# Kernel optimization log

Measured on AMD Instinct MI355X. Metric: run time of the kernel, lower is better.

The kernel has to match this reference:

```python
import jax, jax.numpy as jnp
import numpy as np

DIR_EDGES = [(0,1),(0,2),(0,3),(0,4),(0,13),(0,15),(3,5),(5,6),(4,7),(7,8),(1,9),(9,10),(2,11),(11,12),(13,14),(15,16)]
BP_EDGES = [(1,0),(1,2),(1,3),(1,4),(1,5)]
BODY_PARTS = [[13,14,15,16],[0,3,4],[1,9,10],[2,11,12],[5,6],[7,8]]
V1, V2 = 17, 6           # dir-vec graph nodes, body-part graph nodes
F1 = 16                  # st_gcn output channels
MAX_BP = 4               # max_body_part_edges
NOISE_DIM = 64
EPS = 1e-5


def build_A(num_node, edges, max_hop=2, center=0):
    """ST-GCN 'spatial' partition strategy -> (2*max_hop+1, V, V) float32."""
    adj = np.zeros((num_node, num_node))
    for i, j in edges:
        adj[i, j] = 1.0
        adj[j, i] = 1.0
    hop_dis = np.full((num_node, num_node), np.inf)
    powers = [np.linalg.matrix_power(adj + np.eye(num_node), d) for d in range(max_hop + 1)]
    arrive = np.stack(powers) > 0
    for d in range(max_hop, -1, -1):
        hop_dis[arrive[d]] = d
    adjacency = np.zeros((num_node, num_node))
    for hop in range(max_hop + 1):
        adjacency[hop_dis == hop] = 1.0
    Dl = adjacency.sum(0)
    Dn = np.zeros((num_node, num_node))
    for i in range(num_node):
        if Dl[i] > 0:
            Dn[i, i] = Dl[i] ** -1
    na = adjacency @ Dn
    parts = []
    for hop in range(max_hop + 1):
        a_root = np.zeros((num_node, num_node))
        a_close = np.zeros_like(a_root)
        a_far = np.zeros_like(a_root)
        for i in range(num_node):
            for j in range(num_node):
                if hop_dis[j, i] == hop:
                    if hop_dis[j, center] == hop_dis[i, center]:
                        a_root[j, i] = na[j, i]
                    elif hop_dis[j, center] > hop_dis[i, center]:
                        a_close[j, i] = na[j, i]
                    else:
                        a_far[j, i] = na[j, i]
        if hop == 0:
            parts.append(a_root)
        else:
            parts.append(a_root + a_close)
            parts.append(a_far)
    return np.stack(parts).astype(np.float32)


def _bn_params(k, c):
    k1, k2, k3, k4 = jax.random.split(k, 4)
    gamma = 1.0 + 0.1 * jax.random.normal(k1, (c,), dtype=jnp.float32)
    beta = 0.1 * jax.random.normal(k2, (c,), dtype=jnp.float32)
    mean = 0.1 * jax.random.normal(k3, (c,), dtype=jnp.float32)
    var = 1.0 + 0.1 * jax.random.uniform(k4, (c,), dtype=jnp.float32)
    return gamma, beta, mean, var


def setup_inputs() -> dict:
    key = jax.random.key(0)
    ks = jax.random.split(key, 12)
    n, t = 16, 2048
    poses = jax.random.normal(ks[0], (n, t, V1 * 3), dtype=jnp.float32)
    A1 = jnp.asarray(build_A(V1, DIR_EDGES, max_hop=2, center=0))  # (5,17,17)
    A2 = jnp.asarray(build_A(V2, BP_EDGES, max_hop=2, center=0))   # (5,6,6)
    K = 5
    w1 = 0.05 * jax.random.normal(ks[1], (F1 * K, 3, 9, 5), dtype=jnp.float32)
    b1 = 0.05 * jax.random.normal(ks[2], (F1 * K,), dtype=jnp.float32)
    w2 = 0.05 * jax.random.normal(ks[3], (F1 * K, MAX_BP * F1, 9, 3), dtype=jnp.float32)
    b2 = 0.05 * jax.random.normal(ks[4], (F1 * K,), dtype=jnp.float32)
    w3 = 0.05 * jax.random.normal(ks[5], (16, F1 * V2, 5), dtype=jnp.float32)
    b3 = 0.05 * jax.random.normal(ks[6], (16,), dtype=jnp.float32)
    w4 = 0.05 * jax.random.normal(ks[7], (NOISE_DIM, 16, 3), dtype=jnp.float32)
    b4 = 0.05 * jax.random.normal(ks[8], (NOISE_DIM,), dtype=jnp.float32)
    g1, be1, m1, v1 = _bn_params(ks[9], F1 * V1)
    g2, be2, m2, v2 = _bn_params(ks[10], F1 * V2)
    kk = jax.random.split(ks[11], 2)
    g3, be3, m3, v3 = _bn_params(kk[0], 16)
    g4, be4, m4, v4 = _bn_params(kk[1], NOISE_DIM)
    return dict(poses=poses, A1=A1, A2=A2, w1=w1, b1=b1, g1=g1, be1=be1, m1=m1, v1=v1,
                w2=w2, b2=b2, g2=g2, be2=be2, m2=m2, v2=v2,
                w3=w3, b3=b3, g3=g3, be3=be3, m3=m3, v3=v3,
                w4=w4, b4=b4, g4=g4, be4=be4, m4=m4, v4=v4)


def _bn(x, g, b, m, v):
    # x: (n, C, t), eval-mode BatchNorm1d
    s = (g * jax.lax.rsqrt(v + EPS))
    return (x - m[None, :, None]) * s[None, :, None] + b[None, :, None]


def _conv2d(x, w, b, pad):
    y = jax.lax.conv_general_dilated(x, w, (1, 1), [(pad[0], pad[0]), (pad[1], pad[1])],
                                     dimension_numbers=('NCHW', 'OIHW', 'NCHW'))
    return y + b[None, :, None, None]


def _conv1d(x, w, b, pad):
    y = jax.lax.conv_general_dilated(x, w, (1,), [(pad, pad)],
                                     dimension_numbers=('NCH', 'OIH', 'NCH'))
    return y + b[None, :, None]


def _leaky(x):
    return jax.nn.leaky_relu(x, 0.01)


def reference(poses, A1, A2, w1, b1, g1, be1, m1, v1, w2, b2, g2, be2, m2, v2,
              w3, b3, g3, be3, m3, v3, w4, b4, g4, be4, m4, v4):
    n, t, _ = poses.shape
    K = A1.shape[0]
    # (n, 3, t, V1)
    x = jnp.transpose(poses.reshape(n, t, V1, 3), (0, 3, 1, 2))
    # st_gcn1: 2D conv over (t, v) then graph-partition einsum
    y = _conv2d(x, w1, b1, (4, 2)).reshape(n, K, F1, t, V1)
    f1 = jnp.einsum('nkctv,kvw->nctw', y, A1)            # (n, F1, t, V1)
    # bn1 on flattened (F1*V1) channels
    z = jnp.transpose(f1, (0, 1, 3, 2)).reshape(n, F1 * V1, t)
    z = _bn(z, g1, be1, m1, v1)
    f1bn = jnp.transpose(z.reshape(n, F1, V1, t), (0, 1, 3, 2))  # (n, F1, t, V1)
    # body-part gather/pad assembly -> (n, t, MAX_BP*F1, V2)
    cols = []
    for idxs in BODY_PARTS:
        g = f1bn[:, :, :, jnp.asarray(idxs)]             # (n, F1, t, L)
        g = jnp.transpose(g, (0, 2, 1, 3)).reshape(n, t, -1)  # (n, t, F1*L)
        cols.append(jnp.pad(g, ((0, 0), (0, 0), (0, MAX_BP * F1 - g.shape[-1]))))
    f2_in = jnp.transpose(jnp.stack(cols, axis=-1), (0, 2, 1, 3))  # (n, 64, t, V2)
    # st_gcn2
    y2 = _conv2d(f2_in, w2, b2, (4, 1)).reshape(n, K, F1, t, V2)
    f2 = jnp.einsum('nkctv,kvw->nctw', y2, A2)           # (n, F1, t, V2)
    z2 = jnp.transpose(f2, (0, 1, 3, 2)).reshape(n, F1 * V2, t)
    z2 = _bn(z2, g2, be2, m2, v2)
    f2bn = jnp.transpose(z2.reshape(n, F1, V2, t), (0, 1, 3, 2))   # (n, F1, t, V2)
    # (n, F1*V2, t)
    f3_in = jnp.transpose(jnp.transpose(f2bn, (0, 2, 1, 3)).reshape(n, t, -1), (0, 2, 1))
    f3 = _leaky(_bn(_conv1d(f3_in, w3, b3, 2), g3, be3, m3, v3))
    f4 = _leaky(_bn(_conv1d(f3, w4, b4, 1), g4, be4, m4, v4))
    return jnp.transpose(f4, (0, 2, 1))                  # (n, t, noise_dim)
```

## Files before the change

### kernel.cpp

```cpp
#include <hip/hip_runtime.h>
#include <stdint.h>

typedef unsigned short u16;
typedef __attribute__((ext_vector_type(8))) __bf16 bf16x8;
typedef __attribute__((ext_vector_type(8))) u16 u16x8;
typedef __attribute__((ext_vector_type(4))) float f32x4;

#define T_LEN 2048
#define NB 16

__device__ __forceinline__ u16 f2bf(float f){
  uint32_t x = __builtin_bit_cast(uint32_t, f);
  x += 0x7FFFu + ((x >> 16) & 1u);
  return (u16)(x >> 16);
}

__constant__ int c_part[17] = {1,2,3,1,1,4,4,5,5,2,2,3,3,0,0,0,0};
__constant__ int c_pidx[17] = {0,0,0,1,2,0,1,0,1,1,2,1,2,0,1,2,3};
__constant__ int c_plen[17] = {3,3,3,3,3,2,2,2,2,3,3,3,3,4,4,4,4};

__global__ void prep_all(
  const float* __restrict__ w1, const float* __restrict__ A1, const float* __restrict__ g1, const float* __restrict__ v1, u16* __restrict__ W1f,
  const float* __restrict__ w2, const float* __restrict__ A2, const float* __restrict__ g2, const float* __restrict__ v2, u16* __restrict__ W2f,
  const float* __restrict__ w3, const float* __restrict__ g3, const float* __restrict__ v3, u16* __restrict__ W3f,
  const float* __restrict__ w4, const float* __restrict__ g4, const float* __restrict__ v4, u16* __restrict__ W4f,
  const float* b1, const float* be1, const float* m1,
  const float* b2, const float* be2, const float* m2,
  const float* b3, const float* be3, const float* m3,
  const float* b4, const float* be4, const float* m4,
  float* bias1f, float* bias2f, float* bias3f, float* bias4f)
{
  const int bid = blockIdx.x;
  if (bid < 544){
    int idx = bid * 256 + threadIdx.x;
    int cw = idx >> 9, kp = idx & 511;
    int c = cw / 17, w = cw - c * 17;
    int dt = kp / 56, r0 = kp - dt * 56;
    float val = 0.f;
    if (dt < 9 && r0 < 51){
      int u = r0 / 3, ci = r0 - u * 3;
      for (int kk = 0; kk < 5; ++kk)
        for (int dv = 0; dv < 5; ++dv){
          int v = u - dv + 2;
          if (v >= 0 && v < 17)
            val += w1[(kk*16 + c)*135 + ci*45 + dt*5 + dv] * A1[kk*289 + v*17 + w];
        }
      val *= g1[cw] * rsqrtf(v1[cw] + 1e-5f);
    }
    int mt = cw >> 4, r = cw & 15, ks = kp >> 5, kq = kp & 31;
    W1f[(ks*17 + mt)*512 + ((kq>>3)*16 + r)*8 + (kq&7)] = f2bf(val);
  } else if (bid < 1480){
    int idx = (bid - 544) * 256 + threadIdx.x;
    int cw = idx / 2496, kp = idx - cw * 2496;
    int c = cw / 6, w = cw - c * 6;
    int dt = kp / 272, fj = kp - dt * 272;
    float val = 0.f;
    if (dt < 9){
      int f = fj / 17, J = fj - f * 17;
      int p = c_part[J];
      int ci = f * c_plen[J] + c_pidx[J];
      for (int kk = 0; kk < 5; ++kk)
        for (int dv = 0; dv < 3; ++dv){
          int v = p - dv + 1;
          if (v >= 0 && v < 6)
            val += w2[(kk*16 + c)*1728 + ci*27 + dt*3 + dv] * A2[kk*36 + v*6 + w];
        }
      val *= g2[cw] * rsqrtf(v2[cw] + 1e-5f);
    }
    int mt = cw >> 4, r = cw & 15, ks = kp >> 5, kq = kp & 31;
    W2f[(ks*6 + mt)*512 + ((kq>>3)*16 + r)*8 + (kq&7)] = f2bf(val);
  } else {
    int idx = (bid - 1480) * 256 + threadIdx.x;
    if (idx < 8192){
      int cw = idx >> 9, kp = idx & 511;
      int dt = kp / 96, ch = kp - dt * 96;
      float val = 0.f;
      if (dt < 5){
        float s = g3[cw] * rsqrtf(v3[cw] + 1e-5f);
        val = s * w3[cw*480 + ch*5 + dt];
      }
      int ks = kp >> 5, kq = kp & 31;
      W3f[ks*512 + ((kq>>3)*16 + cw)*8 + (kq&7)] = f2bf(val);
    } else if (idx < 12288){
      int i2 = idx - 8192;
      int cw = i2 >> 6, kp = i2 & 63;
      int dt = kp >> 4, ch = kp & 15;
      float val = 0.f;
      if (dt < 3){
        float s = g4[cw] * rsqrtf(v4[cw] + 1e-5f);
        val = s * w4[cw*48 + ch*3 + dt];
      }
      int mt = cw >> 4, r = cw & 15, ks = kp >> 5, kq = kp & 31;
      W4f[(ks*4 + mt)*512 + ((kq>>3)*16 + r)*8 + (kq&7)] = f2bf(val);
    } else if (idx < 12736){
      int tid = idx - 12288;
      if (tid < 272){
        int c = tid / 17, w = tid - c * 17;
        float beff = 0.f;
        for (int kk = 0; kk < 5; ++kk){
          float rs = 0.f;
          for (int v = 0; v < 17; ++v) rs += A1[kk*289 + v*17 + w];
          beff += b1[kk*16 + c] * rs;
        }
        float s = g1[tid] * rsqrtf(v1[tid] + 1e-5f);
        bias1f[tid] = s * (beff - m1[tid]) + be1[tid];
      } else if (tid < 368){
        int cw = tid - 272;
        int c = cw / 6, w = cw - c * 6;
        float beff = 0.f;
        for (int kk = 0; kk < 5; ++kk){
          float rs = 0.f;
          for (int v = 0; v < 6; ++v) rs += A2[kk*36 + v*6 + w];
          beff += b2[kk*16 + c] * rs;
        }
        float s = g2[cw] * rsqrtf(v2[cw] + 1e-5f);
        bias2f[cw] = s * (beff - m2[cw]) + be2[cw];
      } else if (tid < 384){
        int o = tid - 368;
        float s = g3[o] * rsqrtf(v3[o] + 1e-5f);
        bias3f[o] = s * (b3[o] - m3[o]) + be3[o];
      } else if (tid < 448){
        int o = tid - 384;
        float s = g4[o] * rsqrtf(v4[o] + 1e-5f);
        bias4f[o] = s * (b4[o] - m4[o]) + be4[o];
      }
    }
  }
}

template<int MT, int NW, int NM, int KSTEPS, int RD, int PITCH, int SRC_R, bool IN_F32>
__launch_bounds__(NW*64)
__global__ void gemm_big(const void* __restrict__ src, const u16* __restrict__ Wf,
                         const float* __restrict__ bias, u16* __restrict__ dst)
{
  constexpr int MTOT = MT * 16;
  constexpr int ROWS = 76;
  constexpr int NTH = NW * 64;
  __shared__ u16 patch[ROWS * PITCH];
  const int t0 = blockIdx.x * 64;
  const int n  = blockIdx.y;
  const int tid = threadIdx.x;

  if constexpr (IN_F32){
    for (int idx = tid; idx < ROWS * PITCH; idx += NTH){
      int row = idx / PITCH, col = idx - row * PITCH;
      int ts = t0 + row - 4;
      u16 v = 0;
      if (ts >= 0 && ts < T_LEN && col < SRC_R)
        v = f2bf(((const float*)src)[((size_t)n * T_LEN + ts) * SRC_R + col]);
      patch[idx] = v;
    }
  } else {
    constexpr int GP = PITCH / 8;
    for (int idx = tid; idx < ROWS * GP; idx += NTH){
      int row = idx / GP, g = idx - row * GP;
      int ts = t0 + row - 4;
      int col = g * 8;
      u16x8 v = (u16x8)0;
      if (ts >= 0 && ts < T_LEN && col + 8 <= SRC_R)
        v = *reinterpret_cast<const u16x8*>(&((const u16*)src)[((size_t)n * T_LEN + ts) * SRC_R + col]);
      *reinterpret_cast<u16x8*>(&patch[row * PITCH + col]) = v;
    }
  }
  __syncthreads();

  const int lane = tid & 63;
  const int h    = tid >> 6;
  const int q    = lane >> 4;
  const int l15  = lane & 15;

  bool mok[NM];
  const u16* aptr[NM];
#pragma unroll
  for (int i = 0; i < NM; ++i){
    int mt = h * NM + i;
    mok[i] = (mt < MT);
    aptr[i] = Wf + (size_t)(mok[i] ? mt : 0) * 512 + lane * 8;
  }
  const u16* bp[4];
#pragma unroll
  for (int j = 0; j < 4; ++j)
    bp[j] = patch + (j * 16 + l15) * PITCH;

  f32x4 acc[NM][4];
#pragma unroll
  for (int i = 0; i < NM; ++i)
#pragma unroll
    for (int j = 0; j < 4; ++j)
      acc[i][j] = (f32x4){0.f, 0.f, 0.f, 0.f};

  bf16x8 aF[2][NM];
  bf16x8 bF[2][4];

  auto loadA = [&](int buf, int ks){
    const size_t so = (size_t)ks * (MT * 512);
#pragma unroll
    for (int i = 0; i < NM; ++i)
      aF[buf][i] = *reinterpret_cast<const bf16x8*>(aptr[i] + so);
  };
  auto loadB = [&](int buf, int ks){
    const int k0 = ks * 32 + q * 8;
    const int dt = k0 / RD;
    const int r  = k0 - dt * RD;
    const int od = dt * PITCH + r;
#pragma unroll
    for (int j = 0; j < 4; ++j)
      bF[buf][j] = *reinterpret_cast<const bf16x8*>(bp[j] + od);
  };
  auto step = [&](int buf){
#pragma unroll
    for (int i = 0; i < NM; ++i){
      if (!mok[i]) continue;
#pragma unroll
      for (int j = 0; j < 4; ++j)
        acc[i][j] = __builtin_amdgcn_mfma_f32_16x16x32_bf16(aF[buf][i], bF[buf][j], acc[i][j], 0, 0, 0);
    }
  };

  loadA(0, 0); loadB(0, 0);
  for (int ks = 0; ks + 2 <= KSTEPS; ks += 2){
    loadA(1, ks + 1); loadB(1, ks + 1);
    step(0);
    if (ks + 2 < KSTEPS){ loadA(0, ks + 2); loadB(0, ks + 2); }
    step(1);
  }

#pragma unroll
  for (int i = 0; i < NM; ++i){
    if (!mok[i]) continue;
    const int chb = (h * NM + i) * 16 + q * 4;
    const float b0 = bias[chb+0], b1v = bias[chb+1], b2v = bias[chb+2], b3v = bias[chb+3];
#pragma unroll
    for (int j = 0; j < 4; ++j){
      const int t = t0 + j * 16 + l15;
      ushort4 o;
      o.x = f2bf(acc[i][j][0] + b0);
      o.y = f2bf(acc[i][j][1] + b1v);
      o.z = f2bf(acc[i][j][2] + b2v);
      o.w = f2bf(acc[i][j][3] + b3v);
      *reinterpret_cast<ushort4*>(&dst[((size_t)n * T_LEN + t) * MTOT + chb]) = o;
    }
  }
}

__launch_bounds__(256)
__global__ void gemm34(const u16* __restrict__ X2, const u16* __restrict__ W3f,
                       const float* __restrict__ bias3, const u16* __restrict__ W4f,
                       const float* __restrict__ bias4, float* __restrict__ out)
{
  __shared__ u16 patch[86 * 104];
  __shared__ u16 X3L[80 * 16];
  const int t0 = blockIdx.x * 64;
  const int n  = blockIdx.y;
  const int tid = threadIdx.x;

  for (int idx = tid; idx < 86 * 13; idx += 256){
    int row = idx / 13, g = idx - row * 13;
    int ts = t0 + row - 10;
    int col = g * 8;
    u16x8 v = (u16x8)0;
    if (ts >= 0 && ts < T_LEN && col + 8 <= 96)
      v = *reinterpret_cast<const u16x8*>(&X2[((size_t)n * T_LEN + ts) * 96 + col]);
    *reinterpret_cast<u16x8*>(&patch[row * 104 + col]) = v;
  }
  __syncthreads();

  const int lane = tid & 63;
  const int wv   = tid >> 6;
  const int q    = lane >> 4;
  const int l15  = lane & 15;

  {
    const bool two = (wv == 0);
    f32x4 a0 = (f32x4){0,0,0,0}, a1 = (f32x4){0,0,0,0};
    bf16x8 aF[2], b0F[2], b1F[2];
    const u16* bp0 = patch + (16 * wv + l15) * 104;
    const u16* bp1 = patch + (64 + l15) * 104;
    auto load3 = [&](int buf, int ks){
      const int k0 = ks * 32 + q * 8;
      const int dt = k0 / 96, r = k0 - dt * 96;
      const int od = dt * 104 + r;
      aF[buf]  = *reinterpret_cast<const bf16x8*>(W3f + ks * 512 + lane * 8);
      b0F[buf] = *reinterpret_cast<const bf16x8*>(bp0 + od);
      b1F[buf] = *reinterpret_cast<const bf16x8*>(bp1 + od);
    };
    auto step3 = [&](int buf){
      a0 = __builtin_amdgcn_mfma_f32_16x16x32_bf16(aF[buf], b0F[buf], a0, 0, 0, 0);
      if (two) a1 = __builtin_amdgcn_mfma_f32_16x16x32_bf16(aF[buf], b1F[buf], a1, 0, 0, 0);
    };
    load3(0, 0);
    for (int ks = 0; ks + 2 <= 16; ks += 2){
      load3(1, ks + 1);
      step3(0);
      if (ks + 2 < 16) load3(0, ks + 2);
      step3(1);
    }
    const float c0 = bias3[q*4+0], c1 = bias3[q*4+1], c2 = bias3[q*4+2], c3 = bias3[q*4+3];
    {
      int trow = 16 * wv + l15;
      int t = t0 - 8 + trow;
      float v0 = a0[0]+c0, v1 = a0[1]+c1, v2 = a0[2]+c2, v3 = a0[3]+c3;
      v0 = v0 > 0.f ? v0 : 0.01f*v0; v1 = v1 > 0.f ? v1 : 0.01f*v1;
      v2 = v2 > 0.f ? v2 : 0.01f*v2; v3 = v3 > 0.f ? v3 : 0.01f*v3;
      if (t < 0 || t >= T_LEN){ v0 = v1 = v2 = v3 = 0.f; }
      ushort4 o; o.x = f2bf(v0); o.y = f2bf(v1); o.z = f2bf(v2); o.w = f2bf(v3);
      *reinterpret_cast<ushort4*>(&X3L[trow * 16 + q * 4]) = o;
    }
    if (two){
      int trow = 64 + l15;
      int t = t0 - 8 + trow;
      float v0 = a1[0]+c0, v1 = a1[1]+c1, v2 = a1[2]+c2, v3 = a1[3]+c3;
      v0 = v0 > 0.f ? v0 : 0.01f*v0; v1 = v1 > 0.f ? v1 : 0.01f*v1;
      v2 = v2 > 0.f ? v2 : 0.01f*v2; v3 = v3 > 0.f ? v3 : 0.01f*v3;
      if (t < 0 || t >= T_LEN){ v0 = v1 = v2 = v3 = 0.f; }
      ushort4 o; o.x = f2bf(v0); o.y = f2bf(v1); o.z = f2bf(v2); o.w = f2bf(v3);
      *reinterpret_cast<ushort4*>(&X3L[trow * 16 + q * 4]) = o;
    }
  }
  __syncthreads();

  {
    f32x4 acc[4];
#pragma unroll
    for (int j = 0; j < 4; ++j) acc[j] = (f32x4){0,0,0,0};
    bf16x8 aF[2], bF[2][4];
    auto load4 = [&](int buf, int ks){
      const int k0 = ks * 32 + q * 8;
      const int dt2 = k0 >> 4, ch0 = k0 & 15;
      aF[buf] = *reinterpret_cast<const bf16x8*>(W4f + (ks * 4 + wv) * 512 + lane * 8);
#pragma unroll
      for (int j = 0; j < 4; ++j)
        bF[buf][j] = *reinterpret_cast<const bf16x8*>(&X3L[(j * 16 + l15 + dt2 + 7) * 16 + ch0]);
    };
    load4(0, 0); load4(1, 1);
#pragma unroll
    for (int j = 0; j < 4; ++j)
      acc[j] = __builtin_amdgcn_mfma_f32_16x16x32_bf16(aF[0], bF[0][j], acc[j], 0, 0, 0);
#pragma unroll
    for (int j = 0; j < 4; ++j)
      acc[j] = __builtin_amdgcn_mfma_f32_16x16x32_bf16(aF[1], bF[1][j], acc[j], 0, 0, 0);

    const int chb = wv * 16 + q * 4;
    const float c0 = bias4[chb+0], c1 = bias4[chb+1], c2 = bias4[chb+2], c3 = bias4[chb+3];
#pragma unroll
    for (int j = 0; j < 4; ++j){
      const int t = t0 + j * 16 + l15;
      float v0 = acc[j][0]+c0, v1 = acc[j][1]+c1, v2 = acc[j][2]+c2, v3 = acc[j][3]+c3;
      v0 = v0 > 0.f ? v0 : 0.01f*v0; v1 = v1 > 0.f ? v1 : 0.01f*v1;
      v2 = v2 > 0.f ? v2 : 0.01f*v2; v3 = v3 > 0.f ? v3 : 0.01f*v3;
      float4 o; o.x = v0; o.y = v1; o.z = v2; o.w = v3;
      *reinterpret_cast<float4*>(&out[((size_t)n * T_LEN + t) * 64 + chb]) = o;
    }
  }
}

extern "C" void kernel_launch(void* const* d_in, const int* in_sizes, int n_in,
                              void* d_out, int out_size, void* d_ws, size_t ws_size,
                              hipStream_t stream)
{
  const float* poses = (const float*)d_in[0];
  const float* A1  = (const float*)d_in[1];
  const float* A2  = (const float*)d_in[2];
  const float* w1  = (const float*)d_in[3];
  const float* b1  = (const float*)d_in[4];
  const float* g1  = (const float*)d_in[5];
  const float* be1 = (const float*)d_in[6];
  const float* m1  = (const float*)d_in[7];
  const float* v1  = (const float*)d_in[8];
  const float* w2  = (const float*)d_in[9];
  const float* b2  = (const float*)d_in[10];
  const float* g2  = (const float*)d_in[11];
  const float* be2 = (const float*)d_in[12];
  const float* m2  = (const float*)d_in[13];
  const float* v2  = (const float*)d_in[14];
  const float* w3  = (const float*)d_in[15];
  const float* b3  = (const float*)d_in[16];
  const float* g3  = (const float*)d_in[17];
  const float* be3 = (const float*)d_in[18];
  const float* m3  = (const float*)d_in[19];
  const float* v3  = (const float*)d_in[20];
  const float* w4  = (const float*)d_in[21];
  const float* b4  = (const float*)d_in[22];
  const float* g4  = (const float*)d_in[23];
  const float* be4 = (const float*)d_in[24];
  const float* m4  = (const float*)d_in[25];
  const float* v4  = (const float*)d_in[26];

  uint8_t* ws = (uint8_t*)d_ws;
  size_t off = 0;
  auto alloc = [&](size_t bytes) -> void* {
    void* p = ws + off;
    off += (bytes + 255) & ~(size_t)255;
    return p;
  };
  u16* W1f = (u16*)alloc(16 * 17 * 512 * 2);
  u16* W2f = (u16*)alloc(78 * 6 * 512 * 2);
  u16* W3f = (u16*)alloc(16 * 1 * 512 * 2);
  u16* W4f = (u16*)alloc(2 * 4 * 512 * 2);
  float* bias1f = (float*)alloc(272 * 4);
  float* bias2f = (float*)alloc(96 * 4);
  float* bias3f = (float*)alloc(16 * 4);
  float* bias4f = (float*)alloc(64 * 4);
  u16* X1 = (u16*)alloc((size_t)NB * T_LEN * 272 * 2);
  u16* X2 = (u16*)alloc((size_t)NB * T_LEN * 96 * 2);

  hipLaunchKernelGGL(prep_all, dim3(1530), dim3(256), 0, stream,
                     w1, A1, g1, v1, W1f,
                     w2, A2, g2, v2, W2f,
                     w3, g3, v3, W3f,
                     w4, g4, v4, W4f,
                     b1, be1, m1, b2, be2, m2, b3, be3, m3, b4, be4, m4,
                     bias1f, bias2f, bias3f, bias4f);

  dim3 grid(T_LEN / 64, NB);
  hipLaunchKernelGGL((gemm_big<17, 6, 3, 16, 56, 56, 51, true>), grid, dim3(384), 0, stream,
                     (const void*)poses, W1f, bias1f, X1);
  hipLaunchKernelGGL((gemm_big<6, 3, 2, 78, 272, 280, 272, false>), grid, dim3(192), 0, stream,
                     (const void*)X1, W2f, bias2f, X2);
  hipLaunchKernelGGL(gemm34, grid, dim3(256), 0, stream, X2, W3f, bias3f, W4f, bias4f, (float*)d_out);
}
```

Before: 173.1 us.

## Split GEMM output channels across grid z and halve gemm34 time tile

Replaces the templated gemm_big with two specialized kernels that split output-channel tiles across a new grid z dimension, which doubles the block count and gives each wave fewer M tiles. Stage 2 now computes one M tile per wave with a triple-buffered fragment pipeline. gemm34 uses 32-step time tiles, so it launches twice as many blocks with smaller shared memory. The patch row count is trimmed to the rows actually read. The aim is more parallelism and occupancy, at the cost of each input patch being loaded and converted redundantly by both z blocks.

```diff
diff --git a/kernel.cpp b/kernel.cpp
--- a/kernel.cpp
+++ b/kernel.cpp
@@ -128,39 +128,24 @@
   }
 }
 
-template<int MT, int NW, int NM, int KSTEPS, int RD, int PITCH, int SRC_R, bool IN_F32>
-__launch_bounds__(NW*64)
-__global__ void gemm_big(const void* __restrict__ src, const u16* __restrict__ Wf,
-                         const float* __restrict__ bias, u16* __restrict__ dst)
+__launch_bounds__(192)
+__global__ void gemm_s1(const float* __restrict__ src, const u16* __restrict__ Wf,
+                        const float* __restrict__ bias, u16* __restrict__ dst)
 {
-  constexpr int MTOT = MT * 16;
-  constexpr int ROWS = 76;
-  constexpr int NTH = NW * 64;
+  constexpr int KSTEPS = 16, RD = 56, PITCH = 56, SRC_R = 51, ROWS = 73, NM = 3;
   __shared__ u16 patch[ROWS * PITCH];
   const int t0 = blockIdx.x * 64;
   const int n  = blockIdx.y;
+  const int z  = blockIdx.z;
   const int tid = threadIdx.x;
 
-  if constexpr (IN_F32){
-    for (int idx = tid; idx < ROWS * PITCH; idx += NTH){
-      int row = idx / PITCH, col = idx - row * PITCH;
-      int ts = t0 + row - 4;
-      u16 v = 0;
-      if (ts >= 0 && ts < T_LEN && col < SRC_R)
-        v = f2bf(((const float*)src)[((size_t)n * T_LEN + ts) * SRC_R + col]);
-      patch[idx] = v;
-    }
-  } else {
-    constexpr int GP = PITCH / 8;
-    for (int idx = tid; idx < ROWS * GP; idx += NTH){
-      int row = idx / GP, g = idx - row * GP;
-      int ts = t0 + row - 4;
-      int col = g * 8;
-      u16x8 v = (u16x8)0;
-      if (ts >= 0 && ts < T_LEN && col + 8 <= SRC_R)
-        v = *reinterpret_cast<const u16x8*>(&((const u16*)src)[((size_t)n * T_LEN + ts) * SRC_R + col]);
-      *reinterpret_cast<u16x8*>(&patch[row * PITCH + col]) = v;
-    }
+  for (int idx = tid; idx < ROWS * PITCH; idx += 192){
+    int row = idx / PITCH, col = idx - row * PITCH;
+    int ts = t0 + row - 4;
+    u16 v = 0;
+    if (ts >= 0 && ts < T_LEN && col < SRC_R)
+      v = f2bf(src[((size_t)n * T_LEN + ts) * SRC_R + col]);
+    patch[idx] = v;
   }
   __syncthreads();
 
@@ -173,8 +158,8 @@
   const u16* aptr[NM];
 #pragma unroll
   for (int i = 0; i < NM; ++i){
-    int mt = h * NM + i;
-    mok[i] = (mt < MT);
+    int mt = z * 9 + h * 3 + i;
+    mok[i] = (mt < 17);
     aptr[i] = Wf + (size_t)(mok[i] ? mt : 0) * 512 + lane * 8;
   }
   const u16* bp[4];
@@ -192,13 +177,11 @@
   bf16x8 aF[2][NM];
   bf16x8 bF[2][4];
 
-  auto loadA = [&](int buf, int ks){
-    const size_t so = (size_t)ks * (MT * 512);
+  auto loadstep = [&](int buf, int ks){
+    const size_t so = (size_t)ks * (17 * 512);
 #pragma unroll
     for (int i = 0; i < NM; ++i)
       aF[buf][i] = *reinterpret_cast<const bf16x8*>(aptr[i] + so);
-  };
-  auto loadB = [&](int buf, int ks){
     const int k0 = ks * 32 + q * 8;
     const int dt = k0 / RD;
     const int r  = k0 - dt * RD;
@@ -217,18 +200,18 @@
     }
   };
 
-  loadA(0, 0); loadB(0, 0);
+  loadstep(0, 0);
   for (int ks = 0; ks + 2 <= KSTEPS; ks += 2){
-    loadA(1, ks + 1); loadB(1, ks + 1);
+    loadstep(1, ks + 1);
     step(0);
-    if (ks + 2 < KSTEPS){ loadA(0, ks + 2); loadB(0, ks + 2); }
+    if (ks + 2 < KSTEPS) loadstep(0, ks + 2);
     step(1);
   }
 
 #pragma unroll
   for (int i = 0; i < NM; ++i){
     if (!mok[i]) continue;
-    const int chb = (h * NM + i) * 16 + q * 4;
+    const int chb = (z * 9 + h * 3 + i) * 16 + q * 4;
     const float b0 = bias[chb+0], b1v = bias[chb+1], b2v = bias[chb+2], b3v = bias[chb+3];
 #pragma unroll
     for (int j = 0; j < 4; ++j){
@@ -238,8 +221,91 @@
       o.y = f2bf(acc[i][j][1] + b1v);
       o.z = f2bf(acc[i][j][2] + b2v);
       o.w = f2bf(acc[i][j][3] + b3v);
-      *reinterpret_cast<ushort4*>(&dst[((size_t)n * T_LEN + t) * MTOT + chb]) = o;
-    }
+      *reinterpret_cast<ushort4*>(&dst[((size_t)n * T_LEN + t) * 272 + chb]) = o;
+    }
+  }
+}
+
+__launch_bounds__(192)
+__global__ void gemm_s2(const u16* __restrict__ src, const u16* __restrict__ Wf,
+                        const float* __restrict__ bias, u16* __restrict__ dst)
+{
+  constexpr int KSTEPS = 78, RD = 272, PITCH = 280, SRC_R = 272, ROWS = 73;
+  __shared__ u16 patch[ROWS * PITCH];
+  const int t0 = blockIdx.x * 64;
+  const int n  = blockIdx.y;
+  const int z  = blockIdx.z;
+  const int tid = threadIdx.x;
+
+  constexpr int GP = SRC_R / 8;
+  for (int idx = tid; idx < ROWS * GP; idx += 192){
+    int row = idx / GP, g = idx - row * GP;
+    int ts = t0 + row - 4;
+    int col = g * 8;
+    u16x8 v = (u16x8)0;
+    if (ts >= 0 && ts < T_LEN)
+      v = *reinterpret_cast<const u16x8*>(&src[((size_t)n * T_LEN + ts) * SRC_R + col]);
+    *reinterpret_cast<u16x8*>(&patch[row * PITCH + col]) = v;
+  }
+  __syncthreads();
+
+  const int lane = tid & 63;
+  const int h    = tid >> 6;
+  const int q    = lane >> 4;
+  const int l15  = lane & 15;
+  const int mt   = z * 3 + h;
+
+  const u16* aptr = Wf + (size_t)mt * 512 + lane * 8;
+  const u16* bp[4];
+#pragma unroll
+  for (int j = 0; j < 4; ++j)
+    bp[j] = patch + (j * 16 + l15) * PITCH;
+
+  f32x4 acc[4];
+#pragma unroll
+  for (int j = 0; j < 4; ++j) acc[j] = (f32x4){0.f, 0.f, 0.f, 0.f};
+
+  bf16x8 aF[3];
+  bf16x8 bF[3][4];
+
+  auto loadstep = [&](int buf, int ks){
+    aF[buf] = *reinterpret_cast<const bf16x8*>(aptr + (size_t)ks * (6 * 512));
+    const int k0 = ks * 32 + q * 8;
+    const int dt = k0 / RD;
+    const int r  = k0 - dt * RD;
+    const int od = dt * PITCH + r;
+#pragma unroll
+    for (int j = 0; j < 4; ++j)
+      bF[buf][j] = *reinterpret_cast<const bf16x8*>(bp[j] + od);
+  };
+  auto step = [&](int buf){
+#pragma unroll
+    for (int j = 0; j < 4; ++j)
+      acc[j] = __builtin_amdgcn_mfma_f32_16x16x32_bf16(aF[buf], bF[buf][j], acc[j], 0, 0, 0);
+  };
+
+  loadstep(0, 0);
+  loadstep(1, 1);
+  for (int ks = 0; ks < KSTEPS; ks += 3){
+    loadstep(2, ks + 2);
+    step(0);
+    if (ks + 3 < KSTEPS) loadstep(0, ks + 3);
+    step(1);
+    if (ks + 4 < KSTEPS) loadstep(1, ks + 4);
+    step(2);
+  }
+
+  const int chb = mt * 16 + q * 4;
+  const float b0 = bias[chb+0], b1v = bias[chb+1], b2v = bias[chb+2], b3v = bias[chb+3];
+#pragma unroll
+  for (int j = 0; j < 4; ++j){
+    const int t = t0 + j * 16 + l15;
+    ushort4 o;
+    o.x = f2bf(acc[j][0] + b0);
+    o.y = f2bf(acc[j][1] + b1v);
+    o.z = f2bf(acc[j][2] + b2v);
+    o.w = f2bf(acc[j][3] + b3v);
+    *reinterpret_cast<ushort4*>(&dst[((size_t)n * T_LEN + t) * 96 + chb]) = o;
   }
 }
 
@@ -248,18 +314,18 @@
                        const float* __restrict__ bias3, const u16* __restrict__ W4f,
                        const float* __restrict__ bias4, float* __restrict__ out)
 {
-  __shared__ u16 patch[86 * 104];
-  __shared__ u16 X3L[80 * 16];
-  const int t0 = blockIdx.x * 64;
+  __shared__ u16 patch[53 * 104];
+  __shared__ u16 X3L[48 * 16];
+  const int t0 = blockIdx.x * 32;
   const int n  = blockIdx.y;
   const int tid = threadIdx.x;
 
-  for (int idx = tid; idx < 86 * 13; idx += 256){
-    int row = idx / 13, g = idx - row * 13;
+  for (int idx = tid; idx < 53 * 12; idx += 256){
+    int row = idx / 12, g = idx - row * 12;
     int ts = t0 + row - 10;
     int col = g * 8;
     u16x8 v = (u16x8)0;
-    if (ts >= 0 && ts < T_LEN && col + 8 <= 96)
+    if (ts >= 0 && ts < T_LEN)
       v = *reinterpret_cast<const u16x8*>(&X2[((size_t)n * T_LEN + ts) * 96 + col]);
     *reinterpret_cast<u16x8*>(&patch[row * 104 + col]) = v;
   }
@@ -270,80 +336,60 @@
   const int q    = lane >> 4;
   const int l15  = lane & 15;
 
-  {
-    const bool two = (wv == 0);
-    f32x4 a0 = (f32x4){0,0,0,0}, a1 = (f32x4){0,0,0,0};
-    bf16x8 aF[2], b0F[2], b1F[2];
+  if (wv < 3){
+    f32x4 a0 = (f32x4){0,0,0,0};
+    bf16x8 aF[2], bF[2];
     const u16* bp0 = patch + (16 * wv + l15) * 104;
-    const u16* bp1 = patch + (64 + l15) * 104;
     auto load3 = [&](int buf, int ks){
       const int k0 = ks * 32 + q * 8;
       const int dt = k0 / 96, r = k0 - dt * 96;
-      const int od = dt * 104 + r;
-      aF[buf]  = *reinterpret_cast<const bf16x8*>(W3f + ks * 512 + lane * 8);
-      b0F[buf] = *reinterpret_cast<const bf16x8*>(bp0 + od);
-      b1F[buf] = *reinterpret_cast<const bf16x8*>(bp1 + od);
-    };
-    auto step3 = [&](int buf){
-      a0 = __builtin_amdgcn_mfma_f32_16x16x32_bf16(aF[buf], b0F[buf], a0, 0, 0, 0);
-      if (two) a1 = __builtin_amdgcn_mfma_f32_16x16x32_bf16(aF[buf], b1F[buf], a1, 0, 0, 0);
+      aF[buf] = *reinterpret_cast<const bf16x8*>(W3f + ks * 512 + lane * 8);
+      bF[buf] = *reinterpret_cast<const bf16x8*>(bp0 + dt * 104 + r);
     };
     load3(0, 0);
     for (int ks = 0; ks + 2 <= 16; ks += 2){
       load3(1, ks + 1);
-      step3(0);
+      a0 = __builtin_amdgcn_mfma_f32_16x16x32_bf16(aF[0], bF[0], a0, 0, 0, 0);
       if (ks + 2 < 16) load3(0, ks + 2);
-      step3(1);
+      a0 = __builtin_amdgcn_mfma_f32_16x16x32_bf16(aF[1], bF[1], a0, 0, 0, 0);
     }
     const float c0 = bias3[q*4+0], c1 = bias3[q*4+1], c2 = bias3[q*4+2], c3 = bias3[q*4+3];
-    {
-      int trow = 16 * wv + l15;
-      int t = t0 - 8 + trow;
-      float v0 = a0[0]+c0, v1 = a0[1]+c1, v2 = a0[2]+c2, v3 = a0[3]+c3;
-      v0 = v0 > 0.f ? v0 : 0.01f*v0; v1 = v1 > 0.f ? v1 : 0.01f*v1;
-      v2 = v2 > 0.f ? v2 : 0.01f*v2; v3 = v3 > 0.f ? v3 : 0.01f*v3;
-      if (t < 0 || t >= T_LEN){ v0 = v1 = v2 = v3 = 0.f; }
-      ushort4 o; o.x = f2bf(v0); o.y = f2bf(v1); o.z = f2bf(v2); o.w = f2bf(v3);
-      *reinterpret_cast<ushort4*>(&X3L[trow * 16 + q * 4]) = o;
-    }
-    if (two){
-      int trow = 64 + l15;
-      int t = t0 - 8 + trow;
-      float v0 = a1[0]+c0, v1 = a1[1]+c1, v2 = a1[2]+c2, v3 = a1[3]+c3;
-      v0 = v0 > 0.f ? v0 : 0.01f*v0; v1 = v1 > 0.f ? v1 : 0.01f*v1;
-      v2 = v2 > 0.f ? v2 : 0.01f*v2; v3 = v3 > 0.f ? v3 : 0.01f*v3;
-      if (t < 0 || t >= T_LEN){ v0 = v1 = v2 = v3 = 0.f; }
-      ushort4 o; o.x = f2bf(v0); o.y = f2bf(v1); o.z = f2bf(v2); o.w = f2bf(v3);
-      *reinterpret_cast<ushort4*>(&X3L[trow * 16 + q * 4]) = o;
-    }
+    int trow = 16 * wv + l15;
+    int t = t0 - 8 + trow;
+    float v0 = a0[0]+c0, v1 = a0[1]+c1, v2 = a0[2]+c2, v3 = a0[3]+c3;
+    v0 = v0 > 0.f ? v0 : 0.01f*v0; v1 = v1 > 0.f ? v1 : 0.01f*v1;
+    v2 = v2 > 0.f ? v2 : 0.01f*v2; v3 = v3 > 0.f ? v3 : 0.01f*v3;
+    if (t < 0 || t >= T_LEN){ v0 = v1 = v2 = v3 = 0.f; }
+    ushort4 o; o.x = f2bf(v0); o.y = f2bf(v1); o.z = f2bf(v2); o.w = f2bf(v3);
+    *reinterpret_cast<ushort4*>(&X3L[trow * 16 + q * 4]) = o;
   }
   __syncthreads();
 
   {
-    f32x4 acc[4];
-#pragma unroll
-    for (int j = 0; j < 4; ++j) acc[j] = (f32x4){0,0,0,0};
-    bf16x8 aF[2], bF[2][4];
+    f32x4 acc[2];
+#pragma unroll
+    for (int j = 0; j < 2; ++j) acc[j] = (f32x4){0,0,0,0};
+    bf16x8 aF[2], bF[2][2];
     auto load4 = [&](int buf, int ks){
       const int k0 = ks * 32 + q * 8;
       const int dt2 = k0 >> 4, ch0 = k0 & 15;
       aF[buf] = *reinterpret_cast<const bf16x8*>(W4f + (ks * 4 + wv) * 512 + lane * 8);
 #pragma unroll
-      for (int j = 0; j < 4; ++j)
+      for (int j = 0; j < 2; ++j)
         bF[buf][j] = *reinterpret_cast<const bf16x8*>(&X3L[(j * 16 + l15 + dt2 + 7) * 16 + ch0]);
     };
     load4(0, 0); load4(1, 1);
 #pragma unroll
-    for (int j = 0; j < 4; ++j)
+    for (int j = 0; j < 2; ++j)
       acc[j] = __builtin_amdgcn_mfma_f32_16x16x32_bf16(aF[0], bF[0][j], acc[j], 0, 0, 0);
 #pragma unroll
-    for (int j = 0; j < 4; ++j)
+    for (int j = 0; j < 2; ++j)
       acc[j] = __builtin_amdgcn_mfma_f32_16x16x32_bf16(aF[1], bF[1][j], acc[j], 0, 0, 0);
 
     const int chb = wv * 16 + q * 4;
     const float c0 = bias4[chb+0], c1 = bias4[chb+1], c2 = bias4[chb+2], c3 = bias4[chb+3];
 #pragma unroll
-    for (int j = 0; j < 4; ++j){
+    for (int j = 0; j < 2; ++j){
       const int t = t0 + j * 16 + l15;
       float v0 = acc[j][0]+c0, v1 = acc[j][1]+c1, v2 = acc[j][2]+c2, v3 = acc[j][3]+c3;
       v0 = v0 > 0.f ? v0 : 0.01f*v0; v1 = v1 > 0.f ? v1 : 0.01f*v1;
@@ -412,10 +458,7 @@
                      b1, be1, m1, b2, be2, m2, b3, be3, m3, b4, be4, m4,
                      bias1f, bias2f, bias3f, bias4f);
 
-  dim3 grid(T_LEN / 64, NB);
-  hipLaunchKernelGGL((gemm_big<17, 6, 3, 16, 56, 56, 51, true>), grid, dim3(384), 0, stream,
-                     (const void*)poses, W1f, bias1f, X1);
-  hipLaunchKernelGGL((gemm_big<6, 3, 2, 78, 272, 280, 272, false>), grid, dim3(192), 0, stream,
-                     (const void*)X1, W2f, bias2f, X2);
-  hipLaunchKernelGGL(gemm34, grid, dim3(256), 0, stream, X2, W3f, bias3f, W4f, bias4f, (float*)d_out);
-}
+  hipLaunchKernelGGL(gemm_s1, dim3(32, 16, 2), dim3(192), 0, stream, poses, W1f, bias1f, X1);
+  hipLaunchKernelGGL(gemm_s2, dim3(32, 16, 2), dim3(192), 0, stream, X1, W2f, bias2f, X2);
+  hipLaunchKernelGGL(gemm34, dim3(64, 16), dim3(256), 0, stream, X2, W3f, bias3f, W4f, bias4f, (float*)d_out);
+}
```

Result: faster. 164.6 us (-4.9%).
